# Kernel optimization log

Measured on AMD Instinct MI355X. Metric: run time of the kernel, lower is better.

Reference implementation:

```python
import jax, jax.numpy as jnp
import numpy as np

TEMPERATURE = 8.0  # sqrt(d_head=64)
MASK_FILL = -1e10


def setup_inputs() -> dict:
    key = jax.random.key(0)
    kq, kk, kv, km = jax.random.split(key, 4)
    B, L, D = 64, 2048, 64
    q = jax.random.normal(kq, (B, L, D), dtype=jnp.float32)
    k = jax.random.normal(kk, (B, L, D), dtype=jnp.float32)
    v = jax.random.normal(kv, (B, L, D), dtype=jnp.float32)
    # boolean mask: True means masked-out position (masked_fill semantics)
    mask = jax.random.bernoulli(km, p=0.3, shape=(B, L, L))
    return {"q": q, "k": k, "v": v, "mask": mask}


def reference(q, k, v, mask):
    # attn scores: [B, Lq, Lk]
    attn = jnp.einsum("bqd,bkd->bqk", q, k) / TEMPERATURE
    attn = jnp.where(mask, MASK_FILL, attn)
    attn = jax.nn.softmax(attn, axis=2)
    # dropout is identity in eval/deterministic reference; explain_weight=None
    output = jnp.einsum("bqk,bkd->bqd", attn, v)
    return (output, attn)
```

## Files before the change

kernel.cpp:

```cpp
#include <hip/hip_runtime.h>

typedef __attribute__((ext_vector_type(8))) short short8;
typedef __attribute__((ext_vector_type(4))) float floatx4;
typedef __attribute__((ext_vector_type(4))) float fx4;
typedef __attribute__((ext_vector_type(4))) unsigned ux4;
typedef __attribute__((ext_vector_type(2))) unsigned ux2;

#define B_DIM 64
#define L_SEQ 2048
#define D_H   64
#define BQ    16
#define QK_SCALE 0.1803368801111137f

#define SC_BYTES  (BQ * L_SEQ * 2)
#define RS_OFF    SC_BYTES
#define RI_OFF    (RS_OFF + 64)
#define LDS_TOTAL (RI_OFF + 64)

#if defined(__has_builtin)
#  if __has_builtin(__builtin_amdgcn_exp2f)
#    define EXP2(x) __builtin_amdgcn_exp2f(x)
#  else
#    define EXP2(x) exp2f(x)
#  endif
#else
#  define EXP2(x) exp2f(x)
#endif

__device__ __forceinline__ short f2bf(float f) {
    unsigned u = __builtin_bit_cast(unsigned, f);
    u += 0x7FFFu + ((u >> 16) & 1u);
    return (short)(u >> 16);
}
__device__ __forceinline__ float bf2f_lo(unsigned w) {
    return __builtin_bit_cast(float, w << 16);
}
__device__ __forceinline__ float bf2f_hi(unsigned w) {
    return __builtin_bit_cast(float, w & 0xFFFF0000u);
}
__device__ __forceinline__ unsigned pk2bf(float a, float b) {
    unsigned ua = __builtin_bit_cast(unsigned, a);
    unsigned ub = __builtin_bit_cast(unsigned, b);
    ua += 0x7FFFu + ((ua >> 16) & 1u);
    ub += 0x7FFFu + ((ub >> 16) & 1u);
    return (ua >> 16) | (ub & 0xFFFF0000u);
}
__device__ __forceinline__ int sidx(int row, int colbyte) {
    return row * 4096 + (colbyte ^ ((row & 7) << 4));
}

__global__ __launch_bounds__(256) void prep_qk(const float* __restrict__ q,
                                               const float* __restrict__ k,
                                               unsigned short* __restrict__ qb,
                                               unsigned short* __restrict__ kb) {
    size_t i = (size_t)blockIdx.x * 256 + threadIdx.x;
    fx4 q4 = __builtin_nontemporal_load((const fx4*)q + i);
    fx4 k4 = __builtin_nontemporal_load((const fx4*)k + i);
    ux2 qo, ko;
    qo[0] = pk2bf(q4[0] * QK_SCALE, q4[1] * QK_SCALE);
    qo[1] = pk2bf(q4[2] * QK_SCALE, q4[3] * QK_SCALE);
    ko[0] = pk2bf(k4[0], k4[1]);
    ko[1] = pk2bf(k4[2], k4[3]);
    *((ux2*)qb + i) = qo;
    *((ux2*)kb + i) = ko;
}

__global__ __launch_bounds__(256) void prep_vt(const float* __restrict__ v,
                                               unsigned short* __restrict__ vt) {
    __shared__ float tile[64][65];
    const int b  = blockIdx.x >> 5;
    const int kc = (blockIdx.x & 31) * 64;
    const int t  = threadIdx.x;
    {
        const int r = t >> 2, c4 = (t & 3) * 16;
        const float* src = v + ((size_t)b * L_SEQ + kc + r) * D_H + c4;
        #pragma unroll
        for (int j = 0; j < 4; ++j) {
            fx4 f = __builtin_nontemporal_load((const fx4*)(src + j * 4));
            tile[r][c4 + j * 4 + 0] = f[0]; tile[r][c4 + j * 4 + 1] = f[1];
            tile[r][c4 + j * 4 + 2] = f[2]; tile[r][c4 + j * 4 + 3] = f[3];
        }
    }
    __syncthreads();
    const int d = t >> 2, kq = (t & 3) * 16;
    ux4 o0, o1;
    o0[0] = pk2bf(tile[kq + 0][d], tile[kq + 1][d]);
    o0[1] = pk2bf(tile[kq + 2][d], tile[kq + 3][d]);
    o0[2] = pk2bf(tile[kq + 4][d], tile[kq + 5][d]);
    o0[3] = pk2bf(tile[kq + 6][d], tile[kq + 7][d]);
    o1[0] = pk2bf(tile[kq + 8][d], tile[kq + 9][d]);
    o1[1] = pk2bf(tile[kq +10][d], tile[kq +11][d]);
    o1[2] = pk2bf(tile[kq +12][d], tile[kq +13][d]);
    o1[3] = pk2bf(tile[kq +14][d], tile[kq +15][d]);
    unsigned short* dst = vt + ((size_t)b * D_H + d) * L_SEQ + kc + kq;
    *(ux4*)dst = o0;
    *(ux4*)(dst + 8) = o1;
}

template <bool PRE>
__global__ __launch_bounds__(512, 4)
void sdpa_kernel(const float* __restrict__ qf, const float* __restrict__ kf,
                 const float* __restrict__ vf32, const void* __restrict__ mask,
                 const unsigned short* __restrict__ qb,
                 const unsigned short* __restrict__ kb,
                 const unsigned short* __restrict__ vt,
                 float* __restrict__ out, float* __restrict__ attn)
{
    extern __shared__ char lds[];
    float* s_rsum = (float*)(lds + RS_OFF);
    float* s_rinv = (float*)(lds + RI_OFF);

    const int tid  = threadIdx.x;
    const int wave = tid >> 6;
    const int lane = tid & 63;
    const int l16  = lane & 15;
    const int l4   = lane >> 4;

    const int bid  = blockIdx.x;
    const int sbid = (bid & 7) * 1024 + (bid >> 3);
    const int b     = sbid >> 7;
    const int qbase = (sbid & 127) * BQ;

    const unsigned* mwords = (const unsigned*)mask;
    bool wordMode = true;
    #pragma unroll 8
    for (int i = 0; i < 64; ++i) {
        unsigned w = mwords[i];
        if (!(w == 0u || w == 1u || w == 0x3F800000u)) wordMode = false;
    }

    short8 aq0, aq1;
    if constexpr (PRE) {
        const unsigned short* qrow = qb + ((size_t)b * L_SEQ + qbase + l16) * D_H + l4 * 8;
        aq0 = *(const short8*)(qrow);
        aq1 = *(const short8*)(qrow + 32);
    } else {
        const float* qrow = qf + ((size_t)b * L_SEQ + qbase + l16) * D_H + l4 * 8;
        #pragma unroll
        for (int h = 0; h < 2; ++h) {
            float4 f0 = *(const float4*)(qrow + h * 32);
            float4 f1 = *(const float4*)(qrow + h * 32 + 4);
            short8 a;
            a[0] = f2bf(f0.x * QK_SCALE); a[1] = f2bf(f0.y * QK_SCALE);
            a[2] = f2bf(f0.z * QK_SCALE); a[3] = f2bf(f0.w * QK_SCALE);
            a[4] = f2bf(f1.x * QK_SCALE); a[5] = f2bf(f1.y * QK_SCALE);
            a[6] = f2bf(f1.z * QK_SCALE); a[7] = f2bf(f1.w * QK_SCALE);
            if (h == 0) aq0 = a; else aq1 = a;
        }
    }
    for (int t = 0; t < 16; ++t) {
        const int kt = wave * 16 + t;
        floatx4 c = {0.f, 0.f, 0.f, 0.f};
        if constexpr (PRE) {
            const unsigned short* krow = kb + ((size_t)b * L_SEQ + kt * 16 + l16) * D_H + l4 * 8;
            short8 b0 = *(const short8*)(krow);
            short8 b1 = *(const short8*)(krow + 32);
            c = __builtin_amdgcn_mfma_f32_16x16x32_bf16(aq0, b0, c, 0, 0, 0);
            c = __builtin_amdgcn_mfma_f32_16x16x32_bf16(aq1, b1, c, 0, 0, 0);
        } else {
            const float* krow = kf + ((size_t)b * L_SEQ + kt * 16 + l16) * D_H + l4 * 8;
            #pragma unroll
            for (int h = 0; h < 2; ++h) {
                float4 f0 = *(const float4*)(krow + h * 32);
                float4 f1 = *(const float4*)(krow + h * 32 + 4);
                short8 bk;
                bk[0] = f2bf(f0.x); bk[1] = f2bf(f0.y); bk[2] = f2bf(f0.z); bk[3] = f2bf(f0.w);
                bk[4] = f2bf(f1.x); bk[5] = f2bf(f1.y); bk[6] = f2bf(f1.z); bk[7] = f2bf(f1.w);
                c = __builtin_amdgcn_mfma_f32_16x16x32_bf16(h ? aq1 : aq0, bk, c, 0, 0, 0);
            }
        }
        #pragma unroll
        for (int r = 0; r < 4; ++r)
            *(short*)(lds + sidx(l4 * 4 + r, (kt * 16 + l16) * 2)) = f2bf(c[r]);
    }
    __syncthreads();

    const int qa = tid >> 5;
    const int ca = tid & 31;
    const size_t rowbase = ((size_t)b * L_SEQ + qbase + qa) * (size_t)L_SEQ;

    ux4 ev[8];
    float psum = 0.f;
    if (!wordMode) {
        ux2 mm[8];
        #pragma unroll
        for (int j = 0; j < 8; ++j)
            mm[j] = __builtin_nontemporal_load(
                (const ux2*)((const unsigned char*)mask + rowbase + ca * 8 + j * 256));
        #pragma unroll
        for (int j = 0; j < 8; ++j) {
            const int col = ca * 8 + j * 256;
            ux4 sw = *(ux4*)(lds + sidx(qa, col * 2));
            float e0 = EXP2(bf2f_lo(sw[0])), e1 = EXP2(bf2f_hi(sw[0]));
            float e2 = EXP2(bf2f_lo(sw[1])), e3 = EXP2(bf2f_hi(sw[1]));
            float e4 = EXP2(bf2f_lo(sw[2])), e5 = EXP2(bf2f_hi(sw[2]));
            float e6 = EXP2(bf2f_lo(sw[3])), e7 = EXP2(bf2f_hi(sw[3]));
            unsigned mx = mm[j][0], my = mm[j][1];
            e0 = (mx & 0x000000FFu) ? 0.f : e0;
            e1 = (mx & 0x0000FF00u) ? 0.f : e1;
            e2 = (mx & 0x00FF0000u) ? 0.f : e2;
            e3 = (mx & 0xFF000000u) ? 0.f : e3;
            e4 = (my & 0x000000FFu) ? 0.f : e4;
            e5 = (my & 0x0000FF00u) ? 0.f : e5;
            e6 = (my & 0x00FF0000u) ? 0.f : e6;
            e7 = (my & 0xFF000000u) ? 0.f : e7;
            psum += ((e0 + e1) + (e2 + e3)) + ((e4 + e5) + (e6 + e7));
            ev[j][0] = pk2bf(e0, e1); ev[j][1] = pk2bf(e2, e3);
            ev[j][2] = pk2bf(e4, e5); ev[j][3] = pk2bf(e6, e7);
            *(ux4*)(lds + sidx(qa, col * 2)) = ev[j];
        }
    } else {
        #pragma unroll 2
        for (int j = 0; j < 8; ++j) {
            const int col = ca * 8 + j * 256;
            ux4 sw = *(ux4*)(lds + sidx(qa, col * 2));
            const unsigned* mp = mwords + rowbase + col;
            ux4 ma = __builtin_nontemporal_load((const ux4*)mp);
            ux4 mb = __builtin_nontemporal_load((const ux4*)mp + 1);
            float e0 = EXP2(bf2f_lo(sw[0])), e1 = EXP2(bf2f_hi(sw[0]));
            float e2 = EXP2(bf2f_lo(sw[1])), e3 = EXP2(bf2f_hi(sw[1]));
            float e4 = EXP2(bf2f_lo(sw[2])), e5 = EXP2(bf2f_hi(sw[2]));
            float e6 = EXP2(bf2f_lo(sw[3])), e7 = EXP2(bf2f_hi(sw[3]));
            e0 = ma[0] ? 0.f : e0; e1 = ma[1] ? 0.f : e1;
            e2 = ma[2] ? 0.f : e2; e3 = ma[3] ? 0.f : e3;
            e4 = mb[0] ? 0.f : e4; e5 = mb[1] ? 0.f : e5;
            e6 = mb[2] ? 0.f : e6; e7 = mb[3] ? 0.f : e7;
            psum += ((e0 + e1) + (e2 + e3)) + ((e4 + e5) + (e6 + e7));
            ev[j][0] = pk2bf(e0, e1); ev[j][1] = pk2bf(e2, e3);
            ev[j][2] = pk2bf(e4, e5); ev[j][3] = pk2bf(e6, e7);
            *(ux4*)(lds + sidx(qa, col * 2)) = ev[j];
        }
    }
    #pragma unroll
    for (int off = 1; off < 32; off <<= 1) psum += __shfl_xor(psum, off, 64);
    if (ca == 0) s_rsum[qa] = psum;
    __syncthreads();
    if (tid < 16) s_rinv[tid] = 1.0f / s_rsum[tid];
    __syncthreads();

    {
        const float ri = s_rinv[qa];
        float* arow = attn + rowbase;
        #pragma unroll 2
        for (int j = 0; j < 8; ++j) {
            const int col = ca * 8 + j * 256;
            fx4 o0, o1;
            o0[0] = bf2f_lo(ev[j][0]) * ri; o0[1] = bf2f_hi(ev[j][0]) * ri;
            o0[2] = bf2f_lo(ev[j][1]) * ri; o0[3] = bf2f_hi(ev[j][1]) * ri;
            o1[0] = bf2f_lo(ev[j][2]) * ri; o1[1] = bf2f_hi(ev[j][2]) * ri;
            o1[2] = bf2f_lo(ev[j][3]) * ri; o1[3] = bf2f_hi(ev[j][3]) * ri;
            __builtin_nontemporal_store(o0, (fx4*)(arow + col));
            __builtin_nontemporal_store(o1, (fx4*)(arow + col + 4));
        }
    }

    const int dg = wave & 3;
    const int kh = wave >> 2;
    floatx4 oacc = {0.f, 0.f, 0.f, 0.f};

    if constexpr (PRE) {
        const unsigned short* vtb = vt + ((size_t)b * D_H + dg * 16 + l16) * L_SEQ + kh * 32 + l4 * 8;
        #pragma unroll 4
        for (int ch = 0; ch < 32; ++ch) {
            short8 vfr = *(const short8*)(vtb + ch * 64);
            short8 pf  = *(short8*)(lds + sidx(l16, ch * 128 + kh * 64 + l4 * 16));
            oacc = __builtin_amdgcn_mfma_f32_16x16x32_bf16(pf, vfr, oacc, 0, 0, 0);
        }
    } else {
        const float* vp0 = vf32 + ((size_t)b * L_SEQ + kh * 32 + l4 * 8) * D_H + dg * 16 + l16;
        for (int ch = 0; ch < 32; ++ch) {
            const float* vp = vp0 + (size_t)ch * 64 * D_H;
            short8 vfr;
            #pragma unroll
            for (int i = 0; i < 8; ++i) vfr[i] = f2bf(vp[i * D_H]);
            short8 pf = *(short8*)(lds + sidx(l16, ch * 128 + kh * 64 + l4 * 16));
            oacc = __builtin_amdgcn_mfma_f32_16x16x32_bf16(pf, vfr, oacc, 0, 0, 0);
        }
    }

    __syncthreads();
    float* s_ored = (float*)lds;
    #pragma unroll
    for (int r = 0; r < 4; ++r)
        s_ored[kh * 1024 + (l4 * 4 + r) * 64 + dg * 16 + l16] = oacc[r];
    __syncthreads();
    if (tid < 256) {
        const int qo = tid >> 4, dc = tid & 15;
        float4 a = *(float4*)(s_ored + qo * 64 + dc * 4);
        float4 c = *(float4*)(s_ored + 1024 + qo * 64 + dc * 4);
        const float ri = s_rinv[qo];
        fx4 o;
        o[0] = (a.x + c.x) * ri; o[1] = (a.y + c.y) * ri;
        o[2] = (a.z + c.z) * ri; o[3] = (a.w + c.w) * ri;
        __builtin_nontemporal_store(o, (fx4*)(out + ((size_t)b * L_SEQ + qbase + qo) * D_H + dc * 4));
    }
}

extern "C" void kernel_launch(void* const* d_in, const int* in_sizes, int n_in,
                              void* d_out, int out_size, void* d_ws, size_t ws_size,
                              hipStream_t stream) {
    const float* q = (const float*)d_in[0];
    const float* k = (const float*)d_in[1];
    const float* v = (const float*)d_in[2];
    const void* mask = d_in[3];
    float* out  = (float*)d_out;
    float* attn = out + (size_t)B_DIM * L_SEQ * D_H;

    const size_t NE = (size_t)B_DIM * L_SEQ * D_H;
    dim3 grid(B_DIM * (L_SEQ / BQ), 1, 1);
    dim3 block(512, 1, 1);

    if (ws_size >= NE * 2 * 3) {
        unsigned short* qb = (unsigned short*)d_ws;
        unsigned short* kb = qb + NE;
        unsigned short* vt = kb + NE;
        hipLaunchKernelGGL(prep_qk, dim3(8192), dim3(256), 0, stream, q, k, qb, kb);
        hipLaunchKernelGGL(prep_vt, dim3(2048), dim3(256), 0, stream, v, vt);
        hipLaunchKernelGGL((sdpa_kernel<true>), grid, block, LDS_TOTAL, stream,
                           q, k, v, mask, qb, kb, vt, out, attn);
    } else {
        hipLaunchKernelGGL((sdpa_kernel<false>), grid, block, LDS_TOTAL, stream,
                           q, k, v, mask, (const unsigned short*)nullptr,
                           (const unsigned short*)nullptr, (const unsigned short*)nullptr,
                           out, attn);
    }
}
```

Baseline: 831.1 us.

## Prefetch mask before QK, drop row-sum barriers, double-buffer V loads

Moves the byte-mask loads to the start of the kernel so their latency overlaps the QK^T MFMA phase. Each thread now computes the reciprocal row sum directly from its shuffle-reduced sum, which removes two block barriers. The PV loop software-pipelines V fragment loads four chunks ahead, and the output reduction uses a separate LDS region so it no longer needs the barrier before it. Nontemporal stores become plain stores, and some unroll pragmas change. The cost is more live registers (the mask is held across the QK phase) and a larger LDS footprint, which could hurt occupancy at 4 blocks per CU.

```diff
diff --git a/kernel.cpp b/kernel.cpp
--- a/kernel.cpp
+++ b/kernel.cpp
@@ -13,8 +13,8 @@
 #define QK_SCALE 0.1803368801111137f
 
 #define SC_BYTES  (BQ * L_SEQ * 2)
-#define RS_OFF    SC_BYTES
-#define RI_OFF    (RS_OFF + 64)
+#define CB_OFF    SC_BYTES
+#define RI_OFF    (CB_OFF + 8192)
 #define LDS_TOTAL (RI_OFF + 64)
 
 #if defined(__has_builtin)
@@ -107,7 +107,6 @@
                  float* __restrict__ out, float* __restrict__ attn)
 {
     extern __shared__ char lds[];
-    float* s_rsum = (float*)(lds + RS_OFF);
     float* s_rinv = (float*)(lds + RI_OFF);
 
     const int tid  = threadIdx.x;
@@ -127,6 +126,18 @@
     for (int i = 0; i < 64; ++i) {
         unsigned w = mwords[i];
         if (!(w == 0u || w == 1u || w == 0x3F800000u)) wordMode = false;
+    }
+
+    const int qa = tid >> 5;
+    const int ca = tid & 31;
+    const size_t rowbase = ((size_t)b * L_SEQ + qbase + qa) * (size_t)L_SEQ;
+
+    ux2 mm[8];
+    if (!wordMode) {
+        #pragma unroll
+        for (int j = 0; j < 8; ++j)
+            mm[j] = __builtin_nontemporal_load(
+                (const ux2*)((const unsigned char*)mask + rowbase + ca * 8 + j * 256));
     }
 
     short8 aq0, aq1;
@@ -148,6 +159,7 @@
             if (h == 0) aq0 = a; else aq1 = a;
         }
     }
+    #pragma unroll 2
     for (int t = 0; t < 16; ++t) {
         const int kt = wave * 16 + t;
         floatx4 c = {0.f, 0.f, 0.f, 0.f};
@@ -175,19 +187,10 @@
     }
     __syncthreads();
 
-    const int qa = tid >> 5;
-    const int ca = tid & 31;
-    const size_t rowbase = ((size_t)b * L_SEQ + qbase + qa) * (size_t)L_SEQ;
-
     ux4 ev[8];
     float psum = 0.f;
     if (!wordMode) {
-        ux2 mm[8];
-        #pragma unroll
-        for (int j = 0; j < 8; ++j)
-            mm[j] = __builtin_nontemporal_load(
-                (const ux2*)((const unsigned char*)mask + rowbase + ca * 8 + j * 256));
-        #pragma unroll
+        #pragma unroll 2
         for (int j = 0; j < 8; ++j) {
             const int col = ca * 8 + j * 256;
             ux4 sw = *(ux4*)(lds + sidx(qa, col * 2));
@@ -233,13 +236,10 @@
     }
     #pragma unroll
     for (int off = 1; off < 32; off <<= 1) psum += __shfl_xor(psum, off, 64);
-    if (ca == 0) s_rsum[qa] = psum;
-    __syncthreads();
-    if (tid < 16) s_rinv[tid] = 1.0f / s_rsum[tid];
-    __syncthreads();
+    const float ri = 1.0f / psum;
+    if (ca == 0) s_rinv[qa] = ri;
 
     {
-        const float ri = s_rinv[qa];
         float* arow = attn + rowbase;
         #pragma unroll 2
         for (int j = 0; j < 8; ++j) {
@@ -249,10 +249,11 @@
             o0[2] = bf2f_lo(ev[j][1]) * ri; o0[3] = bf2f_hi(ev[j][1]) * ri;
             o1[0] = bf2f_lo(ev[j][2]) * ri; o1[1] = bf2f_hi(ev[j][2]) * ri;
             o1[2] = bf2f_lo(ev[j][3]) * ri; o1[3] = bf2f_hi(ev[j][3]) * ri;
-            __builtin_nontemporal_store(o0, (fx4*)(arow + col));
-            __builtin_nontemporal_store(o1, (fx4*)(arow + col + 4));
-        }
-    }
+            *(fx4*)(arow + col)     = o0;
+            *(fx4*)(arow + col + 4) = o1;
+        }
+    }
+    __syncthreads();
 
     const int dg = wave & 3;
     const int kh = wave >> 2;
@@ -260,11 +261,31 @@
 
     if constexpr (PRE) {
         const unsigned short* vtb = vt + ((size_t)b * D_H + dg * 16 + l16) * L_SEQ + kh * 32 + l4 * 8;
-        #pragma unroll 4
-        for (int ch = 0; ch < 32; ++ch) {
-            short8 vfr = *(const short8*)(vtb + ch * 64);
-            short8 pf  = *(short8*)(lds + sidx(l16, ch * 128 + kh * 64 + l4 * 16));
-            oacc = __builtin_amdgcn_mfma_f32_16x16x32_bf16(pf, vfr, oacc, 0, 0, 0);
+        short8 vb0 = *(const short8*)(vtb);
+        short8 vb1 = *(const short8*)(vtb + 64);
+        short8 vb2 = *(const short8*)(vtb + 128);
+        short8 vb3 = *(const short8*)(vtb + 192);
+        for (int cc = 0; cc < 8; ++cc) {
+            short8 vn0, vn1, vn2, vn3;
+            if (cc < 7) {
+                const unsigned short* vp = vtb + (cc + 1) * 256;
+                vn0 = *(const short8*)(vp);
+                vn1 = *(const short8*)(vp + 64);
+                vn2 = *(const short8*)(vp + 128);
+                vn3 = *(const short8*)(vp + 192);
+            } else {
+                vn0 = vb0; vn1 = vb1; vn2 = vb2; vn3 = vb3;
+            }
+            const int kbase2 = cc * 512 + kh * 64 + l4 * 16;
+            short8 pf0 = *(short8*)(lds + sidx(l16, kbase2));
+            oacc = __builtin_amdgcn_mfma_f32_16x16x32_bf16(pf0, vb0, oacc, 0, 0, 0);
+            short8 pf1 = *(short8*)(lds + sidx(l16, kbase2 + 128));
+            oacc = __builtin_amdgcn_mfma_f32_16x16x32_bf16(pf1, vb1, oacc, 0, 0, 0);
+            short8 pf2 = *(short8*)(lds + sidx(l16, kbase2 + 256));
+            oacc = __builtin_amdgcn_mfma_f32_16x16x32_bf16(pf2, vb2, oacc, 0, 0, 0);
+            short8 pf3 = *(short8*)(lds + sidx(l16, kbase2 + 384));
+            oacc = __builtin_amdgcn_mfma_f32_16x16x32_bf16(pf3, vb3, oacc, 0, 0, 0);
+            vb0 = vn0; vb1 = vn1; vb2 = vn2; vb3 = vn3;
         }
     } else {
         const float* vp0 = vf32 + ((size_t)b * L_SEQ + kh * 32 + l4 * 8) * D_H + dg * 16 + l16;
@@ -278,21 +299,20 @@
         }
     }
 
-    __syncthreads();
-    float* s_ored = (float*)lds;
+    float* s_comb = (float*)(lds + CB_OFF);
     #pragma unroll
     for (int r = 0; r < 4; ++r)
-        s_ored[kh * 1024 + (l4 * 4 + r) * 64 + dg * 16 + l16] = oacc[r];
+        s_comb[kh * 1024 + (l4 * 4 + r) * 64 + dg * 16 + l16] = oacc[r];
     __syncthreads();
     if (tid < 256) {
         const int qo = tid >> 4, dc = tid & 15;
-        float4 a = *(float4*)(s_ored + qo * 64 + dc * 4);
-        float4 c = *(float4*)(s_ored + 1024 + qo * 64 + dc * 4);
-        const float ri = s_rinv[qo];
+        float4 a = *(float4*)(s_comb + qo * 64 + dc * 4);
+        float4 c = *(float4*)(s_comb + 1024 + qo * 64 + dc * 4);
+        const float rio = s_rinv[qo];
         fx4 o;
-        o[0] = (a.x + c.x) * ri; o[1] = (a.y + c.y) * ri;
-        o[2] = (a.z + c.z) * ri; o[3] = (a.w + c.w) * ri;
-        __builtin_nontemporal_store(o, (fx4*)(out + ((size_t)b * L_SEQ + qbase + qo) * D_H + dc * 4));
+        o[0] = (a.x + c.x) * rio; o[1] = (a.y + c.y) * rio;
+        o[2] = (a.z + c.z) * rio; o[3] = (a.w + c.w) * rio;
+        *(fx4*)(out + ((size_t)b * L_SEQ + qbase + qo) * D_H + dc * 4) = o;
     }
 }
 
```

Measured after the change: 812.6 us. 1.02x faster.
